# Performance work log

Hardware: AMD Instinct MI355X
Metric: run time of the kernel (lower is better)

Reference implementation:

```python
import jax, jax.numpy as jnp
import numpy as np

C, NSET, K, GC = 64, 32, 3, 4
G = C // GC          # 16 groups in KBA
FFN = 2 * C          # FFN_Expand * c
INTERC = 32          # min(c, 32)


def conv2d(x, w, b, padding=0, groups=1, dilation=1):
    out = jax.lax.conv_general_dilated(
        x, w, (1, 1), [(padding, padding)] * 2,
        rhs_dilation=(dilation, dilation),
        feature_group_count=groups,
        dimension_numbers=('NCHW', 'OIHW', 'NCHW'))
    return out + b[None, :, None, None]


def layernorm2d(x, w, b, eps=1e-6):
    mu = x.mean(1, keepdims=True)
    var = ((x - mu) ** 2).mean(1, keepdims=True)
    y = (x - mu) / jnp.sqrt(var + eps)
    return w[None, :, None, None] * y + b[None, :, None, None]


def simple_gate(x):
    x1, x2 = jnp.split(x, 2, axis=1)
    return x1 * x2


def kba(x, att, k, g, b, w):
    # x: [B,c,H,W]; att: [B,nset,H,W]; w: [1,nset,c*(c/g)*k^2]; b: [1,nset,c]
    B, c, H, W = x.shape
    nset = att.shape[1]
    KK = k * k
    cg = c // g
    att2 = att.reshape(B, nset, H * W).transpose(0, 2, 1)       # [B,HW,nset]
    bias = att2 @ b[0]                                          # [B,HW,c]
    attk = (att2 @ w[0]).reshape(B, H * W, g, cg, cg * KK)      # per-pixel grouped weights
    pad = k // 2
    xp = jnp.pad(x, ((0, 0), (0, 0), (pad, pad), (pad, pad)))
    # unfold: torch ordering = (c major, kh, kw)
    patches = jnp.stack([xp[:, :, i:i + H, j:j + W]
                         for i in range(k) for j in range(k)], axis=2)  # [B,c,KK,H,W]
    uf = patches.reshape(B, g, cg * KK, H * W).transpose(0, 3, 1, 2)    # [B,HW,g,cg*KK]
    out = jnp.einsum('bpgoi,bpgi->bpgo', attk, uf)                      # [B,HW,g,cg]
    out = out.reshape(B, H * W, c) + bias
    return out.transpose(0, 2, 1).reshape(B, c, H, W)


def setup_inputs() -> dict:
    key = jax.random.key(0)
    ks = jax.random.split(key, 24)
    n = lambda i, shape, s=0.02: jax.random.normal(ks[i], shape, jnp.float32) * s
    B, H, W = 2, 160, 160
    return {
        'inp': jax.random.normal(ks[0], (B, C, H, W), jnp.float32),
        'ln1_w': jnp.ones((C,), jnp.float32), 'ln1_b': jnp.zeros((C,), jnp.float32),
        'ln2_w': jnp.ones((C,), jnp.float32), 'ln2_b': jnp.zeros((C,), jnp.float32),
        'sca_w': n(1, (C, C, 1, 1)), 'sca_b': n(2, (C,)),
        'c11a_w': n(3, (C, C, 1, 1)), 'c11a_b': n(4, (C,)),
        'c11b_w': n(5, (C, 4, 5, 5)), 'c11b_b': n(6, (C,)),   # groups = c//4 = 16
        'c2a_w': n(7, (INTERC, C // INTERC, 3, 3)), 'c2a_b': n(8, (INTERC,)),
        'c2b_w': n(9, (NSET, INTERC // 2, 1, 1)), 'c2b_b': n(10, (NSET,)),
        'conv3_w': n(11, (C, C, 1, 1)), 'conv3_b': n(12, (C,)),
        'conv4_w': n(13, (FFN, C, 1, 1)), 'conv4_b': n(14, (FFN,)),
        'conv5_w': n(15, (C, FFN // 2, 1, 1)), 'conv5_b': n(16, (C,)),
        'kb_w': n(17, (1, NSET, C * (C // G) * K * K)),        # [1,32,2304]
        'kb_b': n(18, (1, NSET, C)),
        'ga1': jnp.full((1, C, 1, 1), 0.01, jnp.float32),
        'attgamma': jnp.full((1, NSET, 1, 1), 0.01, jnp.float32),
        'beta': jnp.full((1, C, 1, 1), 0.01, jnp.float32),
        'gamma': jnp.full((1, C, 1, 1), 0.01, jnp.float32),
    }


def reference(inp, ln1_w, ln1_b, ln2_w, ln2_b, sca_w, sca_b,
              c11a_w, c11a_b, c11b_w, c11b_b, c2a_w, c2a_b, c2b_w, c2b_b,
              conv3_w, conv3_b, conv4_w, conv4_b, conv5_w, conv5_b,
              kb_w, kb_b, ga1, attgamma, beta, gamma):
    x = layernorm2d(inp, ln1_w, ln1_b)
    # squeeze-excite style channel attention (adaptive avg pool -> 1x1 conv)
    sca = conv2d(x.mean((2, 3), keepdims=True), sca_w, sca_b)
    # attention over kernel basis
    att = conv2d(simple_gate(conv2d(x, c2a_w, c2a_b, padding=1, groups=INTERC)),
                 c2b_w, c2b_b) * attgamma
    # unfolded features: 1x1 conv then 5x5 grouped conv (groups=c//4)
    uf = conv2d(conv2d(x, c11a_w, c11a_b), c11b_w, c11b_b, padding=2, groups=C // 4)
    x = kba(uf, att, K, G, kb_b, kb_w) * ga1 + uf
    x = x * sca
    x = conv2d(x, conv3_w, conv3_b)
    y = inp + x * beta
    # FFN
    x = layernorm2d(y, ln2_w, ln2_b)
    x = simple_gate(conv2d(x, conv4_w, conv4_b))
    x = conv2d(x, conv5_w, conv5_b)
    return y + x * gamma
```

## Files before the change

### kernel.cpp

```cpp
#include <hip/hip_runtime.h>
#include <hip/hip_fp16.h>

#define DEVFN __device__ __forceinline__

constexpr int C   = 64;
constexpr int Hh  = 160, Ww = 160, HW = Hh * Ww;
constexpr int B   = 2;
constexpr int P   = B * HW;
constexpr int NSET = 32;

typedef _Float16 f16;
typedef f16   f16x8 __attribute__((ext_vector_type(8)));
typedef float f32x4 __attribute__((ext_vector_type(4)));


__global__ __launch_bounds__(256) void k0_prep(
        const float* __restrict__ kbw, const float* __restrict__ kbb,
        f16* __restrict__ wp) {
    int e = blockIdx.x * 256 + threadIdx.x;
    int j = e & 7, lane = (e >> 3) & 63, c = (e >> 9) & 1,
        mt = (e >> 10) & 7, g = e >> 13;
    int m = lane & 15, q = lane >> 4;
    int row = mt * 16 + m, s = row >> 2, o = row & 3;
    int k = c * 32 + q * 8 + j;
    float v = 0.f;
    if (k < 36)       v = kbw[(size_t)s * 2304 + g * 144 + o * 36 + k];
    else if (k == 36) v = kbb[s * 64 + g * 4 + o];
    wp[e] = (f16)v;
}

__global__ __launch_bounds__(256) void k0c_pack(
        const float* __restrict__ c11aw, const float* __restrict__ conv3w,
        const float* __restrict__ beta, const float* __restrict__ w4,
        const float* __restrict__ lnw, const float* __restrict__ w5,
        const float* __restrict__ gamma, f16* __restrict__ wk) {
    int e = blockIdx.x * 256 + threadIdx.x;
    if (e >= 20480) return;
    int j = e & 7, lane = (e >> 3) & 63, seg = e >> 9;
    int m = lane & 15, q = lane >> 4;
    float v;
    if (seg < 8) {
        int mt = seg >> 1, c = seg & 1, k = c * 32 + q * 8 + j;
        v = c11aw[(mt * 16 + m) * 64 + k];
    } else if (seg < 16) {
        int s3 = seg - 8, mt = s3 >> 1, c = s3 & 1, k = c * 32 + q * 8 + j;
        int co = mt * 16 + m;
        v = conv3w[co * 64 + k] * beta[co];
    } else if (seg < 32) {
        int s3 = seg - 16, mt = s3 >> 1, c = s3 & 1, k = c * 32 + q * 8 + j;
        v = w4[(mt * 16 + m) * 64 + k] * lnw[k];
    } else {
        int s3 = seg - 32, mt = s3 >> 1, c = s3 & 1, k = c * 32 + q * 8 + j;
        int co = mt * 16 + m;
        v = w5[co * 64 + k] * gamma[co];
    }
    wk[e] = (f16)v;
}

__global__ __launch_bounds__(256) void k0d_const(
        const float* __restrict__ conv3b, const float* __restrict__ beta,
        const float* __restrict__ w4, const float* __restrict__ lnb,
        const float* __restrict__ b4, const float* __restrict__ b5,
        const float* __restrict__ gamma, float* __restrict__ cbuf) {
    int tid = threadIdx.x;
    if (tid < 64) {
        cbuf[tid] = conv3b[tid] * beta[tid];
    } else if (tid < 192) {
        int j = tid - 64;
        float a = 0.f;
#pragma unroll 1
        for (int ci = 0; ci < 64; ci++)
            a = fmaf(w4[j * 64 + ci], lnb[ci], a);
        cbuf[tid] = a + b4[j];
    } else {
        int co = tid - 192;
        cbuf[tid] = b5[co] * gamma[co];
    }
}

__global__ __launch_bounds__(64) void k15_ln1u1(
        const float* __restrict__ inp, const float* __restrict__ lnw,
        const float* __restrict__ lnb, const f16* __restrict__ wk,
        const float* __restrict__ c11ab, float* __restrict__ x1,
        float* __restrict__ u1) {
    int tid = threadIdx.x;
    int m = tid & 15, q = tid >> 4;

    f16x8 A[4][2];
#pragma unroll
    for (int mt = 0; mt < 4; mt++)
#pragma unroll
        for (int c = 0; c < 2; c++)
            A[mt][c] = *(const f16x8*)(wk + ((mt * 2 + c) * 64 + tid) * 8);

    float lnwv[16], lnbv[16];
#pragma unroll
    for (int c = 0; c < 2; c++)
#pragma unroll
        for (int j = 0; j < 8; j++) {
            int k = c * 32 + q * 8 + j;
            lnwv[c * 8 + j] = lnw[k];
            lnbv[c * 8 + j] = lnb[k];
        }
    float bco[16];
#pragma unroll
    for (int mt = 0; mt < 4; mt++)
#pragma unroll
        for (int r = 0; r < 4; r++)
            bco[mt * 4 + r] = c11ab[mt * 16 + q * 4 + r];

    const f32x4 zero = {0.f, 0.f, 0.f, 0.f};

    int tile = blockIdx.x;
    {
        int px0 = tile * 16;
        int b = px0 / HW;
        int hw0 = px0 - b * HW;
        const float* ib = inp + (size_t)b * C * HW + hw0 + m;

        float vin[16];
#pragma unroll
        for (int c = 0; c < 2; c++)
#pragma unroll
            for (int j = 0; j < 8; j++)
                vin[c * 8 + j] = ib[(size_t)(c * 32 + q * 8 + j) * HW];

        float s = 0.f, s2 = 0.f;
#pragma unroll
        for (int i = 0; i < 16; i++) { s += vin[i]; s2 += vin[i] * vin[i]; }
        s  += __shfl_xor(s, 16);  s  += __shfl_xor(s, 32);
        s2 += __shfl_xor(s2, 16); s2 += __shfl_xor(s2, 32);
        float mu  = s * (1.f / 64.f);
        float var = fmaxf(s2 * (1.f / 64.f) - mu * mu, 0.f);
        float r   = rsqrtf(var + 1e-6f);

        float* xo = x1 + (size_t)b * C * HW + hw0 + m;
        f16x8 BX[2];
#pragma unroll
        for (int c = 0; c < 2; c++)
#pragma unroll
            for (int j = 0; j < 8; j++) {
                float v = (vin[c * 8 + j] - mu) * r * lnwv[c * 8 + j] + lnbv[c * 8 + j];
                BX[c][j] = (f16)v;
                xo[(size_t)(c * 32 + q * 8 + j) * HW] = v;
            }

        f32x4 acc[4];
#pragma unroll
        for (int mt = 0; mt < 4; mt++) {
            acc[mt] = __builtin_amdgcn_mfma_f32_16x16x32_f16(A[mt][0], BX[0], zero, 0, 0, 0);
            acc[mt] = __builtin_amdgcn_mfma_f32_16x16x32_f16(A[mt][1], BX[1], acc[mt], 0, 0, 0);
        }
        float* uo = u1 + (size_t)b * C * HW + hw0 + m;
#pragma unroll
        for (int mt = 0; mt < 4; mt++)
#pragma unroll
            for (int r2 = 0; r2 < 4; r2++) {
                int co = mt * 16 + q * 4 + r2;
                uo[(size_t)co * HW] = acc[mt][r2] + bco[mt * 4 + r2];
            }
    }
}

__global__ __launch_bounds__(256) void k2_mean(
        const float* __restrict__ x1, float* __restrict__ meanb) {
    int blk = blockIdx.x;
    int bc = blk >> 2, quarter = blk & 3;
    const float* src = x1 + (size_t)bc * HW + quarter * (HW / 4);
    float s = 0.f;
    for (int i = threadIdx.x; i < HW / 4; i += 256) s += src[i];
#pragma unroll
    for (int o = 32; o > 0; o >>= 1) s += __shfl_down(s, o);
    __shared__ float red[4];
    if ((threadIdx.x & 63) == 0) red[threadIdx.x >> 6] = s;
    __syncthreads();
    if (threadIdx.x == 0)
        atomicAdd(&meanb[bc],
                  (red[0] + red[1] + red[2] + red[3]) * (1.f / HW));
}

__global__ __launch_bounds__(256) void k3_sca(
        const float* __restrict__ scaw, const float* __restrict__ scab_,
        const float* __restrict__ meanb, float* __restrict__ sca) {
    int t = threadIdx.x;
    if (t >= 128) return;
    int b = t >> 6, c = t & 63;
    float acc = scab_[c];
#pragma unroll
    for (int k = 0; k < 64; k++)
        acc = fmaf(scaw[c * 64 + k], meanb[b * 64 + k], acc);
    sca[t] = acc;
}

__global__ __launch_bounds__(128) void k4_att2(
        const float* __restrict__ x1, const float* __restrict__ c2aw,
        const float* __restrict__ c2ab, const float* __restrict__ c2bw,
        const float* __restrict__ c2bb, const float* __restrict__ attg,
        float* __restrict__ att) {
    __shared__ float Wf[1184];
    int tid = threadIdx.x;
    for (int e = tid; e < 1184; e += 128) {
        float v;
        if (e < 576)       v = c2aw[e];
        else if (e < 608)  v = c2ab[e - 576];
        else if (e < 1120) v = c2bw[e - 608];
        else if (e < 1152) v = c2bb[e - 1120];
        else               v = attg[e - 1152];
        Wf[e] = v;
    }
    __syncthreads();

    int wv = tid >> 6, lane = tid & 63;
    int i = lane & 15, q = lane >> 4;
    int p = blockIdx.x * 32 + wv * 16 + i;
    int b = p / HW, hw = p % HW, h = hw / Ww, w = hw % Ww;
    const float* xb = x1 + (size_t)b * C * HW;
    bool interior = (h >= 1 && h < Hh - 1 && w >= 1 && w < Ww - 1);

    float t[8];
#pragma unroll
    for (int j = 0; j < 8; j++) {
        int o = q * 8 + j;
        float acc = Wf[576 + o];
#pragma unroll
        for (int k = 0; k < 2; k++) {
            const float* xc = xb + (size_t)(2 * o + k) * HW;
            const float* wr = &Wf[(o * 2 + k) * 9];
            if (interior) {
#pragma unroll
                for (int kh = 0; kh < 3; kh++)
#pragma unroll
                    for (int kw = 0; kw < 3; kw++)
                        acc = fmaf(wr[kh * 3 + kw],
                                   xc[(h + kh - 1) * Ww + (w + kw - 1)], acc);
            } else {
#pragma unroll
                for (int kh = 0; kh < 3; kh++) {
                    int y = h + kh - 1;
#pragma unroll
                    for (int kw = 0; kw < 3; kw++) {
                        int x = w + kw - 1;
                        if ((unsigned)y < (unsigned)Hh && (unsigned)x < (unsigned)Ww)
                            acc = fmaf(wr[kh * 3 + kw], xc[y * Ww + x], acc);
                    }
                }
            }
        }
        t[j] = acc;
    }

    float g_[8], g2_[8];
#pragma unroll
    for (int j = 0; j < 8; j++) g_[j] = t[j] * __shfl_xor(t[j], 32);
#pragma unroll
    for (int j = 0; j < 8; j++) g2_[j] = __shfl_xor(g_[j], 16);
    float glo[8], ghi[8];
    bool hiq = (q & 1);
#pragma unroll
    for (int j = 0; j < 8; j++) {
        glo[j] = hiq ? g2_[j] : g_[j];
        ghi[j] = hiq ? g_[j] : g2_[j];
    }

    float* ad = att + (size_t)b * NSET * HW + hw;
#pragma unroll
    for (int j = 0; j < 8; j++) {
        int s = q * 8 + j;
        float acc = Wf[1120 + s];
        const float* wr = &Wf[608 + s * 16];
#pragma unroll
        for (int c = 0; c < 8; c++) acc = fmaf(wr[c], glo[c], acc);
#pragma unroll
        for (int c = 0; c < 8; c++) acc = fmaf(wr[8 + c], ghi[c], acc);
        ad[(size_t)s * HW] = acc * Wf[1152 + s];
    }
}

__global__ __launch_bounds__(128) void k6_uf(
        const float* __restrict__ u1, const float* __restrict__ w,
        const float* __restrict__ bias, float* __restrict__ uf) {
    __shared__ float wsm[404];
    int blk = blockIdx.x;
    int g   = blk / 100;
    int ublk = blk % 100;
    int tid = threadIdx.x;
    for (int e = tid; e < 400; e += 128) {
        int o = e / 100, rest = e - o * 100, cl = rest / 25, tp = rest - cl * 25;
        wsm[e] = w[(((g * 4 + o) * 4) + cl) * 25 + tp];
    }
    if (tid < 4) wsm[400 + tid] = bias[g * 4 + tid];
    __syncthreads();

    int unit = ublk * 128 + tid;
    int b  = unit / (HW / 4);
    int rr = unit - b * (HW / 4);
    int r4 = rr / Ww, w_ = rr - r4 * Ww;
    int hA = r4 * 4;
    int hw0 = hA * Ww + w_;
    bool interior = (w_ >= 2 && w_ < Ww - 2 && r4 >= 1 && r4 <= 38);

    float acc[16];
#pragma unroll
    for (int i = 0; i < 16; i++) acc[i] = wsm[400 + (i & 3)];

#pragma unroll 1
    for (int cl = 0; cl < 4; cl++) {
        const float* src = u1 + (size_t)(b * C + g * 4 + cl) * HW;
        float tv[40];
        if (interior) {
#pragma unroll
            for (int rrow = 0; rrow < 8; rrow++)
#pragma unroll
                for (int kw = 0; kw < 5; kw++)
                    tv[rrow * 5 + kw] = src[(hA - 2 + rrow) * Ww + (w_ - 2 + kw)];
        } else {
#pragma unroll
            for (int rrow = 0; rrow < 8; rrow++) {
                int y = hA - 2 + rrow;
#pragma unroll
                for (int kw = 0; kw < 5; kw++) {
                    int x = w_ - 2 + kw;
                    tv[rrow * 5 + kw] =
                        ((unsigned)y < (unsigned)Hh && (unsigned)x < (unsigned)Ww)
                            ? src[y * Ww + x] : 0.f;
                }
            }
        }
#pragma unroll
        for (int o = 0; o < 4; o++) {
            const float* wr = &wsm[(o * 4 + cl) * 25];
#pragma unroll
            for (int kh = 0; kh < 5; kh++)
#pragma unroll
                for (int kw = 0; kw < 5; kw++) {
                    float wv = wr[kh * 5 + kw];
                    acc[0 * 4 + o] = fmaf(wv, tv[(kh + 0) * 5 + kw], acc[0 * 4 + o]);
                    acc[1 * 4 + o] = fmaf(wv, tv[(kh + 1) * 5 + kw], acc[1 * 4 + o]);
                    acc[2 * 4 + o] = fmaf(wv, tv[(kh + 2) * 5 + kw], acc[2 * 4 + o]);
                    acc[3 * 4 + o] = fmaf(wv, tv[(kh + 3) * 5 + kw], acc[3 * 4 + o]);
                }
        }
    }
    float* dst = uf + (size_t)(b * C + g * 4) * HW;
#pragma unroll
    for (int o = 0; o < 4; o++)
#pragma unroll
        for (int px = 0; px < 4; px++)
            dst[o * HW + hw0 + px * Ww] = acc[px * 4 + o];
}

constexpr int ATTS = 336;
__global__ __launch_bounds__(256) void k7_mfma2(
        const float* __restrict__ att, const float* __restrict__ uf,
        const f16* __restrict__ wp, const float* __restrict__ ga1,
        const float* __restrict__ sca, float* __restrict__ xmid) {
    __shared__ f16 UF[4 * 4 * 162];
    __shared__ f16 ATT[32 * ATTS];
    int bi  = blockIdx.x;
    int g   = bi / 160;
    int rp  = bi % 160;
    int b   = rp / 80;
    int h0  = (rp % 80) * 2;
    int hw0 = h0 * Ww;
    int tid = threadIdx.x;
    int wv  = tid >> 6, lane = tid & 63;
    int m   = lane & 15, q = lane >> 4;

    for (int e = tid; e < 4 * 4 * 160; e += 256) {
        int cl = e / 640, r = (e / 160) & 3, x = e % 160;
        int y = h0 - 1 + r;
        float v = ((unsigned)y < (unsigned)Hh)
                      ? uf[(size_t)(b * C + g * 4 + cl) * HW + y * Ww + x] : 0.f;
        UF[cl * 648 + r * 162 + 1 + x] = (f16)v;
    }
    if (tid < 16) {
        int cl = tid >> 2, r = tid & 3;
        UF[cl * 648 + r * 162] = (f16)0.f;
        UF[cl * 648 + r * 162 + 161] = (f16)0.f;
    }
    {
        const float* ab = att + (size_t)b * NSET * HW + hw0;
        for (int e = tid; e < 32 * 320; e += 256) {
            int s = e / 320, px = e - s * 320;
            ATT[s * ATTS + px] = (f16)ab[(size_t)s * HW + px];
        }
    }

    f16x8 A[8][2];
    const f16* wpg = wp + (size_t)g * 8 * 2 * 64 * 8;
#pragma unroll
    for (int mt = 0; mt < 8; mt++)
#pragma unroll
        for (int c = 0; c < 2; c++)
            A[mt][c] = *(const f16x8*)(wpg + ((mt * 2 + c) * 64 + lane) * 8);

    int off0[8];
#pragma unroll
    for (int j = 0; j < 8; j++) {
        int i = q * 8 + j;
        int cl = i / 9, rr = i - cl * 9, kh = rr / 3, kw = rr - kh * 3;
        off0[j] = cl * 648 + kh * 162 + kw;
    }
    int off1[4];
#pragma unroll
    for (int j = 0; j < 4; j++) {
        int i = 32 + j;
        int rr = i - 27, kh = rr / 3, kw = rr - kh * 3;
        off1[j] = 3 * 648 + kh * 162 + kw;
    }

    float gav[4], scb[4];
#pragma unroll
    for (int r = 0; r < 4; r++) {
        gav[r] = ga1[g * 4 + r];
        scb[r] = sca[b * 64 + g * 4 + r];
    }

    __syncthreads();
    const f32x4 zero = {0.f, 0.f, 0.f, 0.f};

#pragma unroll 1
    for (int t = wv; t < 20; t += 4) {
        int tr = t / 10, col0 = (t - tr * 10) * 16;
        int tbase = tr * 162 + col0 + m;
        int pxb   = tr * 160 + col0 + m;

        f16x8 B0, B1;
#pragma unroll
        for (int j = 0; j < 8; j++) B0[j] = UF[off0[j] + tbase];
        if (q == 0) {
#pragma unroll
            for (int j = 0; j < 4; j++) B1[j] = UF[off1[j] + tbase];
            B1[4] = (f16)1.f;
            B1[5] = (f16)0.f; B1[6] = (f16)0.f; B1[7] = (f16)0.f;
        } else {
#pragma unroll
            for (int j = 0; j < 8; j++) B1[j] = (f16)0.f;
        }

        f32x4 acc[8];
#pragma unroll
        for (int mt = 0; mt < 8; mt++) {
            acc[mt] = __builtin_amdgcn_mfma_f32_16x16x32_f16(A[mt][0], B0, zero, 0, 0, 0);
            acc[mt] = __builtin_amdgcn_mfma_f32_16x16x32_f16(A[mt][1], B1, acc[mt], 0, 0, 0);
        }

        float o4[4] = {0.f, 0.f, 0.f, 0.f};
#pragma unroll
        for (int mt = 0; mt < 8; mt++) {
            float av = (float)ATT[(mt * 4 + q) * ATTS + pxb];
#pragma unroll
            for (int r = 0; r < 4; r++) o4[r] = fmaf(av, acc[mt][r], o4[r]);
        }
#pragma unroll
        for (int r = 0; r < 4; r++) {
            o4[r] += __shfl_xor(o4[r], 16);
            o4[r] += __shfl_xor(o4[r], 32);
        }
        if (q == 0) {
            int hw = hw0 + pxb;
#pragma unroll
            for (int r = 0; r < 4; r++) {
                int co = g * 4 + r;
                float cf = uf[(size_t)(b * C + co) * HW + hw];
                xmid[(size_t)(b * C + co) * HW + hw] =
                    (o4[r] * gav[r] + cf) * scb[r];
            }
        }
    }
}

__global__ __launch_bounds__(64) void k89_mfma(
        const float* __restrict__ xmid, const float* __restrict__ inp,
        const f16* __restrict__ wk, const float* __restrict__ cbuf,
        float* __restrict__ out) {
    __shared__ float CONST[256];
    __shared__ f16 TBUF[16 * 72];

    int tid = threadIdx.x;
    int m = tid & 15, q = tid >> 4;

    CONST[tid] = cbuf[tid];
    CONST[64 + tid] = cbuf[64 + tid];
    CONST[128 + tid] = cbuf[128 + tid];
    CONST[192 + tid] = cbuf[192 + tid];

    f16x8 A3[4][2], A4[8][2], A5[4][2];
#pragma unroll
    for (int mt = 0; mt < 4; mt++)
#pragma unroll
        for (int c = 0; c < 2; c++) {
            A3[mt][c] = *(const f16x8*)(wk + ((8 + mt * 2 + c) * 64 + tid) * 8);
            A5[mt][c] = *(const f16x8*)(wk + ((32 + mt * 2 + c) * 64 + tid) * 8);
        }
#pragma unroll
    for (int mt = 0; mt < 8; mt++)
#pragma unroll
        for (int c = 0; c < 2; c++)
            A4[mt][c] = *(const f16x8*)(wk + ((16 + mt * 2 + c) * 64 + tid) * 8);
    __syncthreads();

    float c3i[16], b5g[16];
#pragma unroll
    for (int mt = 0; mt < 4; mt++)
#pragma unroll
        for (int r = 0; r < 4; r++) {
            c3i[mt * 4 + r] = CONST[mt * 16 + q * 4 + r];
            b5g[mt * 4 + r] = CONST[192 + mt * 16 + q * 4 + r];
        }

    const f32x4 zero = {0.f, 0.f, 0.f, 0.f};

    int tile = blockIdx.x;
    {
        int px0 = tile * 16;
        int b = px0 / HW;
        int hw0 = px0 - b * HW;
        const float* xb = xmid + (size_t)b * C * HW + hw0 + m;
        const float* ib = inp + (size_t)b * C * HW + hw0 + m;
        float* ob = out + (size_t)b * C * HW + hw0 + m;

        f16x8 BX[2];
#pragma unroll
        for (int c = 0; c < 2; c++)
#pragma unroll
            for (int j = 0; j < 8; j++)
                BX[c][j] = (f16)xb[(size_t)(c * 32 + q * 8 + j) * HW];

        f32x4 accY[4];
#pragma unroll
        for (int mt = 0; mt < 4; mt++) {
            accY[mt] = __builtin_amdgcn_mfma_f32_16x16x32_f16(A3[mt][0], BX[0], zero, 0, 0, 0);
            accY[mt] = __builtin_amdgcn_mfma_f32_16x16x32_f16(A3[mt][1], BX[1], accY[mt], 0, 0, 0);
        }
        float y[16];
#pragma unroll
        for (int mt = 0; mt < 4; mt++)
#pragma unroll
            for (int r = 0; r < 4; r++) {
                int co = mt * 16 + q * 4 + r;
                y[mt * 4 + r] = ib[(size_t)co * HW] + accY[mt][r] + c3i[mt * 4 + r];
            }

        float s = 0.f, s2 = 0.f;
#pragma unroll
        for (int i = 0; i < 16; i++) { s += y[i]; s2 += y[i] * y[i]; }
        s  += __shfl_xor(s, 16);  s  += __shfl_xor(s, 32);
        s2 += __shfl_xor(s2, 16); s2 += __shfl_xor(s2, 32);
        float mu  = s * (1.f / 64.f);
        float var = fmaxf(s2 * (1.f / 64.f) - mu * mu, 0.f);
        float rr  = rsqrtf(var + 1e-6f);

#pragma unroll
        for (int mt = 0; mt < 4; mt++)
#pragma unroll
            for (int r = 0; r < 4; r++)
                TBUF[m * 72 + mt * 16 + q * 4 + r] = (f16)(y[mt * 4 + r] - mu);
        __syncthreads();
        f16x8 BV[2];
#pragma unroll
        for (int c = 0; c < 2; c++)
#pragma unroll
            for (int j = 0; j < 8; j++)
                BV[c][j] = TBUF[m * 72 + c * 32 + q * 8 + j];

        f32x4 accT[8];
#pragma unroll
        for (int mt = 0; mt < 8; mt++) {
            accT[mt] = __builtin_amdgcn_mfma_f32_16x16x32_f16(A4[mt][0], BV[0], zero, 0, 0, 0);
            accT[mt] = __builtin_amdgcn_mfma_f32_16x16x32_f16(A4[mt][1], BV[1], accT[mt], 0, 0, 0);
        }
        __syncthreads();

#pragma unroll
        for (int mt = 0; mt < 4; mt++)
#pragma unroll
            for (int r = 0; r < 4; r++) {
                int j = mt * 16 + q * 4 + r;
                float t1 = rr * accT[mt][r] + CONST[64 + j];
                float t2 = rr * accT[mt + 4][r] + CONST[128 + j];
                TBUF[m * 72 + j] = (f16)(t1 * t2);
            }
        __syncthreads();
        f16x8 BG[2];
#pragma unroll
        for (int c = 0; c < 2; c++)
#pragma unroll
            for (int j = 0; j < 8; j++)
                BG[c][j] = TBUF[m * 72 + c * 32 + q * 8 + j];

        f32x4 accO[4];
#pragma unroll
        for (int mt = 0; mt < 4; mt++) {
            accO[mt] = __builtin_amdgcn_mfma_f32_16x16x32_f16(A5[mt][0], BG[0], zero, 0, 0, 0);
            accO[mt] = __builtin_amdgcn_mfma_f32_16x16x32_f16(A5[mt][1], BG[1], accO[mt], 0, 0, 0);
        }
#pragma unroll
        for (int mt = 0; mt < 4; mt++)
#pragma unroll
            for (int r = 0; r < 4; r++) {
                int co = mt * 16 + q * 4 + r;
                ob[(size_t)co * HW] = y[mt * 4 + r] + accO[mt][r] + b5g[mt * 4 + r];
            }
    }
}

extern "C" void kernel_launch(void* const* d_in, const int* in_sizes, int n_in,
                              void* d_out, int out_size, void* d_ws, size_t ws_size,
                              hipStream_t stream) {
    (void)in_sizes; (void)n_in; (void)out_size; (void)ws_size;

    const float* inp     = (const float*)d_in[0];
    const float* ln1_w   = (const float*)d_in[1];
    const float* ln1_b   = (const float*)d_in[2];
    const float* ln2_w   = (const float*)d_in[3];
    const float* ln2_b   = (const float*)d_in[4];
    const float* sca_w   = (const float*)d_in[5];
    const float* sca_b   = (const float*)d_in[6];
    const float* c11a_w  = (const float*)d_in[7];
    const float* c11a_b  = (const float*)d_in[8];
    const float* c11b_w  = (const float*)d_in[9];
    const float* c11b_b  = (const float*)d_in[10];
    const float* c2a_w   = (const float*)d_in[11];
    const float* c2a_b   = (const float*)d_in[12];
    const float* c2b_w   = (const float*)d_in[13];
    const float* c2b_b   = (const float*)d_in[14];
    const float* conv3_w = (const float*)d_in[15];
    const float* conv3_b = (const float*)d_in[16];
    const float* conv4_w = (const float*)d_in[17];
    const float* conv4_b = (const float*)d_in[18];
    const float* conv5_w = (const float*)d_in[19];
    const float* conv5_b = (const float*)d_in[20];
    const float* kb_w    = (const float*)d_in[21];
    const float* kb_b    = (const float*)d_in[22];
    const float* ga1     = (const float*)d_in[23];
    const float* attg    = (const float*)d_in[24];
    const float* beta    = (const float*)d_in[25];
    const float* gamma   = (const float*)d_in[26];

    char* ws = (char*)d_ws;
    size_t off = 0;
    auto alloc = [&](size_t bytes) {
        void* r = ws + off;
        off += (bytes + 255) & ~(size_t)255;
        return r;
    };
    f16*   wpk   = (f16*)alloc(131072 * 2);
    f16*   wk2   = (f16*)alloc(20480 * 2);
    float* cbuf  = (float*)alloc(256 * 4);
    float* meanb = (float*)alloc(128 * 4);
    float* scab  = (float*)alloc(128 * 4);
    float* x1    = (float*)alloc((size_t)P * 64 * 4);
    float* attb  = (float*)alloc((size_t)P * 32 * 4);
    float* u1    = (float*)alloc((size_t)P * 64 * 4);
    float* ufb   = x1;
    float* xmid  = u1;

    hipMemsetAsync(meanb, 0, 128 * 4, stream);

    k0_prep  <<<512, 256, 0, stream>>>(kb_w, kb_b, wpk);
    k0c_pack <<<80, 256, 0, stream>>>(c11a_w, conv3_w, beta, conv4_w, ln2_w,
                                      conv5_w, gamma, wk2);
    k0d_const<<<1, 256, 0, stream>>>(conv3_b, beta, conv4_w, ln2_b, conv4_b,
                                     conv5_b, gamma, cbuf);
    k15_ln1u1<<<3200, 64, 0, stream>>>(inp, ln1_w, ln1_b, wk2, c11a_b,
                                       x1, u1);
    k2_mean  <<<512, 256, 0, stream>>>(x1, meanb);
    k3_sca   <<<1, 128, 0, stream>>>(sca_w, sca_b, meanb, scab);
    k4_att2  <<<P / 32, 128, 0, stream>>>(x1, c2a_w, c2a_b, c2b_w, c2b_b,
                                          attg, attb);
    k6_uf    <<<1600, 128, 0, stream>>>(u1, c11b_w, c11b_b, ufb);
    k7_mfma2 <<<2560, 256, 0, stream>>>(attb, ufb, wpk, ga1, scab, xmid);
    k89_mfma <<<3200, 64, 0, stream>>>(xmid, inp, wk2, cbuf, (float*)d_out);
}
```

Before: 273.0 us.

## Store intermediate activations in fp16 and load them as packed pairs

The intermediate buffers (x1, u1, att, uf, xmid) change from fp32 to fp16, which halves global memory traffic across every stage of the block. The k7 shared-memory staging now copies fp16 pairs as 32-bit words, with padded strides of 164 and 340 in place of 162 and 336. The tradeoff is lower precision in the intermediates, including the LN1 output feeding the spatial mean and the attention conv, and the residual uf term now passes through fp16.

```diff
diff --git a/kernel.cpp b/kernel.cpp
--- a/kernel.cpp
+++ b/kernel.cpp
@@ -81,8 +81,8 @@
 __global__ __launch_bounds__(64) void k15_ln1u1(
         const float* __restrict__ inp, const float* __restrict__ lnw,
         const float* __restrict__ lnb, const f16* __restrict__ wk,
-        const float* __restrict__ c11ab, float* __restrict__ x1,
-        float* __restrict__ u1) {
+        const float* __restrict__ c11ab, f16* __restrict__ x1,
+        f16* __restrict__ u1) {
     int tid = threadIdx.x;
     int m = tid & 15, q = tid >> 4;
 
@@ -134,7 +134,7 @@
         float var = fmaxf(s2 * (1.f / 64.f) - mu * mu, 0.f);
         float r   = rsqrtf(var + 1e-6f);
 
-        float* xo = x1 + (size_t)b * C * HW + hw0 + m;
+        f16* xo = x1 + (size_t)b * C * HW + hw0 + m;
         f16x8 BX[2];
 #pragma unroll
         for (int c = 0; c < 2; c++)
@@ -142,7 +142,7 @@
             for (int j = 0; j < 8; j++) {
                 float v = (vin[c * 8 + j] - mu) * r * lnwv[c * 8 + j] + lnbv[c * 8 + j];
                 BX[c][j] = (f16)v;
-                xo[(size_t)(c * 32 + q * 8 + j) * HW] = v;
+                xo[(size_t)(c * 32 + q * 8 + j) * HW] = (f16)v;
             }
 
         f32x4 acc[4];
@@ -151,24 +151,24 @@
             acc[mt] = __builtin_amdgcn_mfma_f32_16x16x32_f16(A[mt][0], BX[0], zero, 0, 0, 0);
             acc[mt] = __builtin_amdgcn_mfma_f32_16x16x32_f16(A[mt][1], BX[1], acc[mt], 0, 0, 0);
         }
-        float* uo = u1 + (size_t)b * C * HW + hw0 + m;
+        f16* uo = u1 + (size_t)b * C * HW + hw0 + m;
 #pragma unroll
         for (int mt = 0; mt < 4; mt++)
 #pragma unroll
             for (int r2 = 0; r2 < 4; r2++) {
                 int co = mt * 16 + q * 4 + r2;
-                uo[(size_t)co * HW] = acc[mt][r2] + bco[mt * 4 + r2];
+                uo[(size_t)co * HW] = (f16)(acc[mt][r2] + bco[mt * 4 + r2]);
             }
     }
 }
 
 __global__ __launch_bounds__(256) void k2_mean(
-        const float* __restrict__ x1, float* __restrict__ meanb) {
+        const f16* __restrict__ x1, float* __restrict__ meanb) {
     int blk = blockIdx.x;
     int bc = blk >> 2, quarter = blk & 3;
-    const float* src = x1 + (size_t)bc * HW + quarter * (HW / 4);
+    const f16* src = x1 + (size_t)bc * HW + quarter * (HW / 4);
     float s = 0.f;
-    for (int i = threadIdx.x; i < HW / 4; i += 256) s += src[i];
+    for (int i = threadIdx.x; i < HW / 4; i += 256) s += (float)src[i];
 #pragma unroll
     for (int o = 32; o > 0; o >>= 1) s += __shfl_down(s, o);
     __shared__ float red[4];
@@ -193,10 +193,10 @@
 }
 
 __global__ __launch_bounds__(128) void k4_att2(
-        const float* __restrict__ x1, const float* __restrict__ c2aw,
+        const f16* __restrict__ x1, const float* __restrict__ c2aw,
         const float* __restrict__ c2ab, const float* __restrict__ c2bw,
         const float* __restrict__ c2bb, const float* __restrict__ attg,
-        float* __restrict__ att) {
+        f16* __restrict__ att) {
     __shared__ float Wf[1184];
     int tid = threadIdx.x;
     for (int e = tid; e < 1184; e += 128) {
@@ -214,7 +214,7 @@
     int i = lane & 15, q = lane >> 4;
     int p = blockIdx.x * 32 + wv * 16 + i;
     int b = p / HW, hw = p % HW, h = hw / Ww, w = hw % Ww;
-    const float* xb = x1 + (size_t)b * C * HW;
+    const f16* xb = x1 + (size_t)b * C * HW;
     bool interior = (h >= 1 && h < Hh - 1 && w >= 1 && w < Ww - 1);
 
     float t[8];
@@ -224,7 +224,7 @@
         float acc = Wf[576 + o];
 #pragma unroll
         for (int k = 0; k < 2; k++) {
-            const float* xc = xb + (size_t)(2 * o + k) * HW;
+            const f16* xc = xb + (size_t)(2 * o + k) * HW;
             const float* wr = &Wf[(o * 2 + k) * 9];
             if (interior) {
 #pragma unroll
@@ -232,7 +232,7 @@
 #pragma unroll
                     for (int kw = 0; kw < 3; kw++)
                         acc = fmaf(wr[kh * 3 + kw],
-                                   xc[(h + kh - 1) * Ww + (w + kw - 1)], acc);
+                                   (float)xc[(h + kh - 1) * Ww + (w + kw - 1)], acc);
             } else {
 #pragma unroll
                 for (int kh = 0; kh < 3; kh++) {
@@ -241,7 +241,7 @@
                     for (int kw = 0; kw < 3; kw++) {
                         int x = w + kw - 1;
                         if ((unsigned)y < (unsigned)Hh && (unsigned)x < (unsigned)Ww)
-                            acc = fmaf(wr[kh * 3 + kw], xc[y * Ww + x], acc);
+                            acc = fmaf(wr[kh * 3 + kw], (float)xc[y * Ww + x], acc);
                     }
                 }
             }
@@ -262,7 +262,7 @@
         ghi[j] = hiq ? g_[j] : g2_[j];
     }
 
-    float* ad = att + (size_t)b * NSET * HW + hw;
+    f16* ad = att + (size_t)b * NSET * HW + hw;
 #pragma unroll
     for (int j = 0; j < 8; j++) {
         int s = q * 8 + j;
@@ -272,13 +272,13 @@
         for (int c = 0; c < 8; c++) acc = fmaf(wr[c], glo[c], acc);
 #pragma unroll
         for (int c = 0; c < 8; c++) acc = fmaf(wr[8 + c], ghi[c], acc);
-        ad[(size_t)s * HW] = acc * Wf[1152 + s];
+        ad[(size_t)s * HW] = (f16)(acc * Wf[1152 + s]);
     }
 }
 
 __global__ __launch_bounds__(128) void k6_uf(
-        const float* __restrict__ u1, const float* __restrict__ w,
-        const float* __restrict__ bias, float* __restrict__ uf) {
+        const f16* __restrict__ u1, const float* __restrict__ w,
+        const float* __restrict__ bias, f16* __restrict__ uf) {
     __shared__ float wsm[404];
     int blk = blockIdx.x;
     int g   = blk / 100;
@@ -305,14 +305,14 @@
 
 #pragma unroll 1
     for (int cl = 0; cl < 4; cl++) {
-        const float* src = u1 + (size_t)(b * C + g * 4 + cl) * HW;
+        const f16* src = u1 + (size_t)(b * C + g * 4 + cl) * HW;
         float tv[40];
         if (interior) {
 #pragma unroll
             for (int rrow = 0; rrow < 8; rrow++)
 #pragma unroll
                 for (int kw = 0; kw < 5; kw++)
-                    tv[rrow * 5 + kw] = src[(hA - 2 + rrow) * Ww + (w_ - 2 + kw)];
+                    tv[rrow * 5 + kw] = (float)src[(hA - 2 + rrow) * Ww + (w_ - 2 + kw)];
         } else {
 #pragma unroll
             for (int rrow = 0; rrow < 8; rrow++) {
@@ -322,7 +322,7 @@
                     int x = w_ - 2 + kw;
                     tv[rrow * 5 + kw] =
                         ((unsigned)y < (unsigned)Hh && (unsigned)x < (unsigned)Ww)
-                            ? src[y * Ww + x] : 0.f;
+                            ? (float)src[y * Ww + x] : 0.f;
                 }
             }
         }
@@ -341,21 +341,23 @@
                 }
         }
     }
-    float* dst = uf + (size_t)(b * C + g * 4) * HW;
+    f16* dst = uf + (size_t)(b * C + g * 4) * HW;
 #pragma unroll
     for (int o = 0; o < 4; o++)
 #pragma unroll
         for (int px = 0; px < 4; px++)
-            dst[o * HW + hw0 + px * Ww] = acc[px * 4 + o];
-}
-
-constexpr int ATTS = 336;
+            dst[o * HW + hw0 + px * Ww] = (f16)acc[px * 4 + o];
+}
+
+constexpr int ATTS = 340;
 __global__ __launch_bounds__(256) void k7_mfma2(
-        const float* __restrict__ att, const float* __restrict__ uf,
+        const f16* __restrict__ att, const f16* __restrict__ uf,
         const f16* __restrict__ wp, const float* __restrict__ ga1,
-        const float* __restrict__ sca, float* __restrict__ xmid) {
-    __shared__ f16 UF[4 * 4 * 162];
-    __shared__ f16 ATT[32 * ATTS];
+        const float* __restrict__ sca, f16* __restrict__ xmid) {
+    __shared__ unsigned UFa[4 * 4 * 82];
+    __shared__ unsigned ATTa[32 * 170];
+    f16* UF  = (f16*)UFa;
+    f16* ATT = (f16*)ATTa;
     int bi  = blockIdx.x;
     int g   = bi / 160;
     int rp  = bi % 160;
@@ -366,23 +368,27 @@
     int wv  = tid >> 6, lane = tid & 63;
     int m   = lane & 15, q = lane >> 4;
 
-    for (int e = tid; e < 4 * 4 * 160; e += 256) {
-        int cl = e / 640, r = (e / 160) & 3, x = e % 160;
-        int y = h0 - 1 + r;
-        float v = ((unsigned)y < (unsigned)Hh)
-                      ? uf[(size_t)(b * C + g * 4 + cl) * HW + y * Ww + x] : 0.f;
-        UF[cl * 648 + r * 162 + 1 + x] = (f16)v;
-    }
-    if (tid < 16) {
-        int cl = tid >> 2, r = tid & 3;
-        UF[cl * 648 + r * 162] = (f16)0.f;
-        UF[cl * 648 + r * 162 + 161] = (f16)0.f;
-    }
     {
-        const float* ab = att + (size_t)b * NSET * HW + hw0;
-        for (int e = tid; e < 32 * 320; e += 256) {
-            int s = e / 320, px = e - s * 320;
-            ATT[s * ATTS + px] = (f16)ab[(size_t)s * HW + px];
+        const unsigned* uf32 = (const unsigned*)uf;
+        for (int e = tid; e < 1280; e += 256) {
+            int cl = e / 320, r = (e / 80) & 3, xw = e % 80;
+            int y = h0 - 1 + r;
+            unsigned v = 0u;
+            if ((unsigned)y < (unsigned)Hh)
+                v = uf32[((size_t)(b * C + g * 4 + cl) * HW >> 1) + y * 80 + xw];
+            UFa[cl * 328 + r * 82 + 1 + xw] = v;
+        }
+        if (tid < 32) {
+            int cl = tid >> 3, r = (tid >> 1) & 3, side = tid & 1;
+            UFa[cl * 328 + r * 82 + side * 81] = 0u;
+        }
+    }
+    {
+        const unsigned* ab32 =
+            (const unsigned*)(att + (size_t)b * NSET * HW + hw0);
+        for (int e = tid; e < 5120; e += 256) {
+            int s = e / 160, pw = e % 160;
+            ATTa[s * 170 + pw] = ab32[(size_t)s * (HW >> 1) + pw];
         }
     }
 
@@ -399,14 +405,14 @@
     for (int j = 0; j < 8; j++) {
         int i = q * 8 + j;
         int cl = i / 9, rr = i - cl * 9, kh = rr / 3, kw = rr - kh * 3;
-        off0[j] = cl * 648 + kh * 162 + kw;
+        off0[j] = cl * 656 + kh * 164 + kw;
     }
     int off1[4];
 #pragma unroll
     for (int j = 0; j < 4; j++) {
         int i = 32 + j;
         int rr = i - 27, kh = rr / 3, kw = rr - kh * 3;
-        off1[j] = 3 * 648 + kh * 162 + kw;
+        off1[j] = 3 * 656 + kh * 164 + kw;
     }
 
     float gav[4], scb[4];
@@ -422,7 +428,7 @@
 #pragma unroll 1
     for (int t = wv; t < 20; t += 4) {
         int tr = t / 10, col0 = (t - tr * 10) * 16;
-        int tbase = tr * 162 + col0 + m;
+        int tbase = tr * 164 + col0 + m + 1;
         int pxb   = tr * 160 + col0 + m;
 
         f16x8 B0, B1;
@@ -462,16 +468,16 @@
 #pragma unroll
             for (int r = 0; r < 4; r++) {
                 int co = g * 4 + r;
-                float cf = uf[(size_t)(b * C + co) * HW + hw];
+                float cf = (float)uf[(size_t)(b * C + co) * HW + hw];
                 xmid[(size_t)(b * C + co) * HW + hw] =
-                    (o4[r] * gav[r] + cf) * scb[r];
+                    (f16)((o4[r] * gav[r] + cf) * scb[r]);
             }
         }
     }
 }
 
 __global__ __launch_bounds__(64) void k89_mfma(
-        const float* __restrict__ xmid, const float* __restrict__ inp,
+        const f16* __restrict__ xmid, const float* __restrict__ inp,
         const f16* __restrict__ wk, const float* __restrict__ cbuf,
         float* __restrict__ out) {
     __shared__ float CONST[256];
@@ -516,7 +522,7 @@
         int px0 = tile * 16;
         int b = px0 / HW;
         int hw0 = px0 - b * HW;
-        const float* xb = xmid + (size_t)b * C * HW + hw0 + m;
+        const f16* xb = xmid + (size_t)b * C * HW + hw0 + m;
         const float* ib = inp + (size_t)b * C * HW + hw0 + m;
         float* ob = out + (size_t)b * C * HW + hw0 + m;
 
@@ -525,7 +531,7 @@
         for (int c = 0; c < 2; c++)
 #pragma unroll
             for (int j = 0; j < 8; j++)
-                BX[c][j] = (f16)xb[(size_t)(c * 32 + q * 8 + j) * HW];
+                BX[c][j] = xb[(size_t)(c * 32 + q * 8 + j) * HW];
 
         f32x4 accY[4];
 #pragma unroll
@@ -650,11 +656,11 @@
     float* cbuf  = (float*)alloc(256 * 4);
     float* meanb = (float*)alloc(128 * 4);
     float* scab  = (float*)alloc(128 * 4);
-    float* x1    = (float*)alloc((size_t)P * 64 * 4);
-    float* attb  = (float*)alloc((size_t)P * 32 * 4);
-    float* u1    = (float*)alloc((size_t)P * 64 * 4);
-    float* ufb   = x1;
-    float* xmid  = u1;
+    f16*   x1    = (f16*)alloc((size_t)P * 64 * 2);
+    f16*   attb  = (f16*)alloc((size_t)P * 32 * 2);
+    f16*   u1    = (f16*)alloc((size_t)P * 64 * 2);
+    f16*   ufb   = x1;
+    f16*   xmid  = u1;
 
     hipMemsetAsync(meanb, 0, 128 * 4, stream);
 
```

New measurement: 277.9 us. About the same (+1.8%).
